# Kernel optimization log

Hardware: AMD Instinct MI355X
Metric: run time of the kernel (lower is better)

The kernel has to match this reference:

```python
import jax, jax.numpy as jnp
import numpy as np

B, V = 4, 10242
N = B * V            # 40968 packed vertices
E_PER = 30720        # edges per mesh
HID = 128


def _bilinear_sample(fm, grid):
    """pytorch3d vert_align core: grid_sample(align_corners=True, bilinear).
    fm: [B,C,H,W], grid: [B,V,2] xy in [-1,1] -> [B,V,C]."""
    b_, c_, h_, w_ = fm.shape
    x = (grid[..., 0] + 1.0) * 0.5 * (w_ - 1)
    y = (grid[..., 1] + 1.0) * 0.5 * (h_ - 1)
    x0f, y0f = jnp.floor(x), jnp.floor(y)
    wx1, wy1 = x - x0f, y - y0f
    wx0, wy0 = 1.0 - wx1, 1.0 - wy1
    x0 = jnp.clip(x0f, 0, w_ - 1).astype(jnp.int32)
    x1 = jnp.clip(x0f + 1, 0, w_ - 1).astype(jnp.int32)
    y0 = jnp.clip(y0f, 0, h_ - 1).astype(jnp.int32)
    y1 = jnp.clip(y0f + 1, 0, h_ - 1).astype(jnp.int32)
    fmt = jnp.transpose(fm, (0, 2, 3, 1))  # [B,H,W,C]
    bi = jnp.arange(b_)[:, None]
    g = lambda yy, xx: fmt[bi, yy, xx]     # [B,V,C]
    return ((wy0 * wx0)[..., None] * g(y0, x0)
            + (wy0 * wx1)[..., None] * g(y0, x1)
            + (wy1 * wx0)[..., None] * g(y1, x0)
            + (wy1 * wx1)[..., None] * g(y1, x1))


def _graph_conv(x, edges, w0, b0, w1, b1):
    """pytorch3d GraphConv (undirected): W0 x_i + sum over both edge dirs of W1 x_j."""
    h0 = x @ w0 + b0
    h1 = x @ w1 + b1
    e0, e1 = edges[:, 0], edges[:, 1]
    agg = jnp.zeros_like(h0).at[e0].add(h1[e1]).at[e1].add(h1[e0])
    return h0 + agg


def setup_inputs() -> dict:
    key = jax.random.key(0)
    ks = jax.random.split(key, 20)
    s = 0.05
    # per-mesh edges, offset into packed index space
    e = jax.random.randint(ks[0], (B, E_PER, 2), 0, V)
    e = e + (jnp.arange(B) * V)[:, None, None]
    return {
        "feat1": jax.random.normal(ks[1], (B, 256, 56, 56), jnp.float32),
        "feat2": jax.random.normal(ks[2], (B, 512, 28, 28), jnp.float32),
        "feat3": jax.random.normal(ks[3], (B, 1024, 14, 14), jnp.float32),
        "feat4": jax.random.normal(ks[4], (B, 2048, 7, 7), jnp.float32),
        "aligned_verts": jax.random.uniform(ks[5], (B, V, 3), jnp.float32, -1.0, 1.0),
        "verts_packed": jax.random.normal(ks[6], (N, 3), jnp.float32),
        "image_enc": jax.random.normal(ks[7], (B, 256), jnp.float32),
        "edges": e.reshape(B * E_PER, 2).astype(jnp.int64),
        "bottleneck_w": jax.random.normal(ks[8], (3840, HID), jnp.float32) * s,
        "bottleneck_b": jnp.zeros((HID,), jnp.float32),
        "g0_w0": jax.random.normal(ks[9], (387, HID), jnp.float32) * s,
        "g0_b0": jnp.zeros((HID,), jnp.float32),
        "g0_w1": jax.random.normal(ks[10], (387, HID), jnp.float32) * s,
        "g0_b1": jnp.zeros((HID,), jnp.float32),
        "gw0": jax.random.normal(ks[11], (7, HID, HID), jnp.float32) * s,
        "gb0": jnp.zeros((7, HID), jnp.float32),
        "gw1": jax.random.normal(ks[12], (7, HID, HID), jnp.float32) * s,
        "gb1": jnp.zeros((7, HID), jnp.float32),
        "off_w": jax.random.normal(ks[13], (HID, 3), jnp.float32) * s,
        "off_b": jnp.zeros((3,), jnp.float32),
    }


def reference(feat1, feat2, feat3, feat4, aligned_verts, verts_packed, image_enc,
              edges, bottleneck_w, bottleneck_b, g0_w0, g0_b0, g0_w1, g0_b1,
              gw0, gb0, gw1, gb1, off_w, off_b):
    grid = aligned_verts[..., :2]  # vert_align uses xy only
    samp = jnp.concatenate([_bilinear_sample(f, grid)
                            for f in (feat1, feat2, feat3, feat4)], axis=-1)
    samp = samp.reshape(N, 3840)  # return_packed=True
    vfeat = jax.nn.relu(samp @ bottleneck_w + bottleneck_b)
    enc = jnp.repeat(image_enc, V, axis=0)  # repeat_interleave
    x = jnp.concatenate([vfeat, verts_packed, enc], axis=1)  # [N,387]
    x = jax.nn.relu(_graph_conv(x, edges, g0_w0, g0_b0, g0_w1, g0_b1))
    for i in range(7):
        x = jax.nn.relu(_graph_conv(x, edges, gw0[i], gb0[i], gw1[i], gb1[i]))
    return x @ off_w + off_b  # delta_v [N,3]
```

## Files before the change

kernel.cpp:

```cpp
#include <hip/hip_runtime.h>

static inline int ceil_div(int a, int b) { return (a + b - 1) / b; }

typedef __attribute__((ext_vector_type(8))) short short8;
typedef __attribute__((ext_vector_type(4))) float floatx4;

__device__ __forceinline__ unsigned short f2bf(float f) {
    unsigned int u = __float_as_uint(f);
    unsigned int r = (u + 0x7fffu + ((u >> 16) & 1u)) >> 16;
    return (unsigned short)r;
}
__device__ __forceinline__ float bf2f(unsigned short h) {
    return __uint_as_float(((unsigned int)h) << 16);
}

__global__ __launch_bounds__(1024) void scan1_k(const int* __restrict__ deg,
                                                int* __restrict__ excl,
                                                int* __restrict__ bsum, int Nv) {
    __shared__ int s[1024];
    int tid = threadIdx.x;
    int i = blockIdx.x * 1024 + tid;
    int v = (i < Nv) ? deg[i] : 0;
    s[tid] = v;
    __syncthreads();
    for (int off = 1; off < 1024; off <<= 1) {
        int t = (tid >= off) ? s[tid - off] : 0;
        __syncthreads();
        if (tid >= off) s[tid] += t;
        __syncthreads();
    }
    if (i < Nv) excl[i] = s[tid] - v;
    if (tid == 1023) bsum[blockIdx.x] = s[1023];
}

__global__ __launch_bounds__(64) void scan2_k(int* __restrict__ bsum, int nb) {
    __shared__ int s[64];
    int tid = threadIdx.x;
    int v = (tid < nb) ? bsum[tid] : 0;
    s[tid] = v;
    __syncthreads();
    for (int off = 1; off < 64; off <<= 1) {
        int t = (tid >= off) ? s[tid - off] : 0;
        __syncthreads();
        if (tid >= off) s[tid] += t;
        __syncthreads();
    }
    if (tid < nb) bsum[tid] = s[tid] - v;
}

__global__ __launch_bounds__(1024) void scan3_k(const int* __restrict__ excl,
                                                const int* __restrict__ bsum,
                                                const int* __restrict__ deg,
                                                int* __restrict__ rowptr,
                                                int* __restrict__ cursor, int Nv) {
    int i = blockIdx.x * 1024 + threadIdx.x;
    if (i < Nv) {
        int val = excl[i] + bsum[blockIdx.x];
        rowptr[i] = val;
        cursor[i] = val;
        if (i == Nv - 1) rowptr[Nv] = val + deg[i];
    }
}

__global__ __launch_bounds__(256) void fill_adj_k(const int* __restrict__ edges,
                                                  int* __restrict__ cursor,
                                                  int* __restrict__ adj, int E) {
    int e = blockIdx.x * blockDim.x + threadIdx.x;
    if (e < E) {
        int a = edges[2 * e], b = edges[2 * e + 1];
        adj[atomicAdd(&cursor[a], 1)] = b;
        adj[atomicAdd(&cursor[b], 1)] = a;
    }
}

__global__ __launch_bounds__(256) void fatpre_k(const int* __restrict__ edges,
                                                int* __restrict__ deg, int E, int nE,
                                                const float* __restrict__ g0w0,
                                                const float* __restrict__ g0w1,
                                                const float* __restrict__ gw0,
                                                const float* __restrict__ gw1,
                                                unsigned short* __restrict__ Wt,
                                                const float* __restrict__ enc,
                                                float* __restrict__ encp, int B_) {
    int bid = blockIdx.x;
    int tid = threadIdx.x;
    if (bid < nE) {
        int e = bid * 256 + tid;
        if (e < E) {
            atomicAdd(&deg[edges[2 * e]], 1);
            atomicAdd(&deg[edges[2 * e + 1]], 1);
        }
    } else if (bid < nE + 16) {
        int lh = bid - nE;
        int l = lh >> 1, h = lh & 1;
        const float* src;
        if (l == 0) src = h ? g0w1 : g0w0;
        else src = (h ? gw1 : gw0) + (size_t)(l - 1) * 16384;
        unsigned short* dst = Wt + (size_t)lh * 16384;
        for (int idx = tid; idx < 16384; idx += 256) {
            int n = idx >> 7, k = idx & 127;
            dst[n * 128 + k] = f2bf(src[k * 128 + n]);
        }
    } else {
        int b = bid - nE - 16;
        int sH = tid >> 7;
        int j = tid & 127;
        const float* w = sH ? g0w1 : g0w0;
        const float* eb = enc + b * 256;
        float acc = 0.f;
        for (int c = 0; c < 256; ++c) acc = fmaf(eb[c], w[(131 + c) * 128 + j], acc);
        encp[(sH * B_ + b) * 128 + j] = acc;
    }
}

__global__ __launch_bounds__(256) void proj_all_k(
    const float* __restrict__ fm1, const float* __restrict__ fm2,
    const float* __restrict__ fm3, const float* __restrict__ fm4,
    const float* __restrict__ bw, float* __restrict__ q1, float* __restrict__ q2,
    float* __restrict__ q3, float* __restrict__ q4, int B_) {
    __shared__ float Xs[32][64];
    __shared__ float Ws[32][128];
    int tid = threadIdx.x;

    int n1 = 49 * B_ * 4, n2 = 13 * B_ * 8, n3 = 4 * B_ * 16;
    int bid = blockIdx.x;
    const float* fm;
    const float* W;
    float* op;
    int C, HW, PT, idx;
    if (bid < n1) {
        fm = fm1; W = bw; op = q1; C = 256; HW = 3136; PT = 49; idx = bid;
    } else if (bid < n1 + n2) {
        fm = fm2; W = bw + 256 * 128; op = q2; C = 512; HW = 784; PT = 13; idx = bid - n1;
    } else if (bid < n1 + n2 + n3) {
        fm = fm3; W = bw + 768 * 128; op = q3; C = 1024; HW = 196; PT = 4; idx = bid - n1 - n2;
    } else {
        fm = fm4; W = bw + 1792 * 128; op = q4; C = 2048; HW = 49; PT = 1;
        idx = bid - n1 - n2 - n3;
    }
    int pt = idx % PT;
    int r2 = idx / PT;
    int b = r2 % B_;
    int zz = r2 / B_;
    int p0 = pt * 64;
    int c0 = zz * 64;
    int S = B_ * HW * 128;
    const float* fmb = fm + (size_t)b * C * HW;

    float acc[8][4];
#pragma unroll
    for (int i = 0; i < 8; i++)
#pragma unroll
        for (int j = 0; j < 4; j++) acc[i][j] = 0.f;

    bool vec_ok = ((HW & 3) == 0);
    for (int kc = c0; kc < c0 + 64; kc += 32) {
        {
            int p4 = (tid & 15) * 4;
            int k0 = tid >> 4;
#pragma unroll
            for (int kk = 0; kk < 32; kk += 16) {
                int k = k0 + kk;
                const float* src = fmb + (size_t)(kc + k) * HW + p0 + p4;
                float4 v;
                if (vec_ok && (p0 + p4 + 3 < HW)) {
                    v = *(const float4*)src;
                } else {
                    v.x = (p0 + p4 + 0 < HW) ? src[0] : 0.f;
                    v.y = (p0 + p4 + 1 < HW) ? src[1] : 0.f;
                    v.z = (p0 + p4 + 2 < HW) ? src[2] : 0.f;
                    v.w = (p0 + p4 + 3 < HW) ? src[3] : 0.f;
                }
                *(float4*)&Xs[k][p4] = v;
            }
        }
        {
            int j4 = (tid & 31) * 4;
            int k0 = tid >> 5;
#pragma unroll
            for (int kk = 0; kk < 32; kk += 8) {
                int k = k0 + kk;
                *(float4*)&Ws[k][j4] = *(const float4*)(W + (size_t)(kc + k) * 128 + j4);
            }
        }
        __syncthreads();
        int rb = (tid >> 5) * 8;
        int cb = (tid & 31) * 4;
#pragma unroll 8
        for (int k = 0; k < 32; ++k) {
            float xr[8], wc[4];
#pragma unroll
            for (int i = 0; i < 8; i++) xr[i] = Xs[k][rb + i];
#pragma unroll
            for (int j = 0; j < 4; j++) wc[j] = Ws[k][cb + j];
#pragma unroll
            for (int i = 0; i < 8; i++)
#pragma unroll
                for (int j = 0; j < 4; j++) acc[i][j] = fmaf(xr[i], wc[j], acc[i][j]);
        }
        __syncthreads();
    }
    int rb = (tid >> 5) * 8;
    int cb = (tid & 31) * 4;
    float* obase = op + (size_t)zz * S;
#pragma unroll
    for (int i = 0; i < 8; i++) {
        int p = p0 + rb + i;
        if (p < HW) {
            *(float4*)(obase + ((size_t)b * HW + p) * 128 + cb) =
                make_float4(acc[i][0], acc[i][1], acc[i][2], acc[i][3]);
        }
    }
}

__global__ __launch_bounds__(256) void reduce4_k(const float* __restrict__ q1,
                                                 const float* __restrict__ q2,
                                                 const float* __restrict__ q3,
                                                 const float* __restrict__ q4,
                                                 float* __restrict__ o1, float* __restrict__ o2,
                                                 float* __restrict__ o3, float* __restrict__ o4,
                                                 int S1, int S2, int S3, int S4) {
    int i = (blockIdx.x * 256 + threadIdx.x) * 4;
    const float* src;
    float* dst;
    int S, z, base;
    if (i < S1) {
        src = q1; dst = o1; S = S1; z = 4; base = i;
    } else if (i < S1 + S2) {
        src = q2; dst = o2; S = S2; z = 8; base = i - S1;
    } else if (i < S1 + S2 + S3) {
        src = q3; dst = o3; S = S3; z = 16; base = i - S1 - S2;
    } else if (i < S1 + S2 + S3 + S4) {
        src = q4; dst = o4; S = S4; z = 32; base = i - S1 - S2 - S3;
    } else {
        return;
    }
    float4 a = *(const float4*)(src + base);
    for (int zz = 1; zz < z; ++zz) {
        float4 b = *(const float4*)(src + (size_t)zz * S + base);
        a.x += b.x; a.y += b.y; a.z += b.z; a.w += b.w;
    }
    *(float4*)(dst + base) = a;
}

__device__ __forceinline__ float sample_level(const float* __restrict__ pp, int Hh, int Ww,
                                              float gx, float gy, int j) {
    float x = (gx + 1.f) * 0.5f * (float)(Ww - 1);
    float y = (gy + 1.f) * 0.5f * (float)(Hh - 1);
    float x0f = floorf(x), y0f = floorf(y);
    float wx1 = x - x0f, wy1 = y - y0f;
    float wx0 = 1.f - wx1, wy0 = 1.f - wy1;
    int x0 = (int)fminf(fmaxf(x0f, 0.f), (float)(Ww - 1));
    int x1 = (int)fminf(fmaxf(x0f + 1.f, 0.f), (float)(Ww - 1));
    int y0 = (int)fminf(fmaxf(y0f, 0.f), (float)(Hh - 1));
    int y1 = (int)fminf(fmaxf(y0f + 1.f, 0.f), (float)(Hh - 1));
    const float* r00 = pp + (size_t)(y0 * Ww + x0) * 128;
    const float* r01 = pp + (size_t)(y0 * Ww + x1) * 128;
    const float* r10 = pp + (size_t)(y1 * Ww + x0) * 128;
    const float* r11 = pp + (size_t)(y1 * Ww + x1) * 128;
    return wy0 * (wx0 * r00[j] + wx1 * r01[j]) + wy1 * (wx0 * r10[j] + wx1 * r11[j]);
}

__global__ __launch_bounds__(128) void sample_bottleneck_k(
    const float* __restrict__ av, const float* __restrict__ pp1, const float* __restrict__ pp2,
    const float* __restrict__ pp3, const float* __restrict__ pp4, const float* __restrict__ bb,
    const float* __restrict__ verts, const float* __restrict__ encp,
    const float* __restrict__ g0w0, const float* __restrict__ g0w1,
    const float* __restrict__ g0b0, const float* __restrict__ g0b1,
    unsigned short* __restrict__ X, unsigned short* __restrict__ H, int V_, int B_) {
    int n = blockIdx.x, j = threadIdx.x;
    int b = n / V_;
    float gx = av[(size_t)n * 3 + 0];
    float gy = av[(size_t)n * 3 + 1];
    float acc = bb[j];
    acc += sample_level(pp1 + (size_t)b * 3136 * 128, 56, 56, gx, gy, j);
    acc += sample_level(pp2 + (size_t)b * 784 * 128, 28, 28, gx, gy, j);
    acc += sample_level(pp3 + (size_t)b * 196 * 128, 14, 14, gx, gy, j);
    acc += sample_level(pp4 + (size_t)b * 49 * 128, 7, 7, gx, gy, j);
    X[(size_t)n * 128 + j] = f2bf(fmaxf(acc, 0.f));
    float v0 = verts[n * 3 + 0], v1 = verts[n * 3 + 1], v2 = verts[n * 3 + 2];
    float h0 = encp[(0 * B_ + b) * 128 + j] + g0b0[j] + v0 * g0w0[128 * 128 + j] +
               v1 * g0w0[129 * 128 + j] + v2 * g0w0[130 * 128 + j];
    float h1 = encp[(1 * B_ + b) * 128 + j] + g0b1[j] + v0 * g0w1[128 * 128 + j] +
               v1 * g0w1[129 * 128 + j] + v2 * g0w1[130 * 128 + j];
    H[(size_t)n * 256 + j] = f2bf(h0);
    H[(size_t)n * 256 + 128 + j] = f2bf(h1);
}

__global__ __launch_bounds__(256) void aggpre_k(const unsigned short* __restrict__ H,
                                                const int* __restrict__ rowptr,
                                                const int* __restrict__ adj,
                                                float* __restrict__ pre, int Nv) {
    int wave = threadIdx.x >> 6, lane = threadIdx.x & 63;
    int n = blockIdx.x * 4 + wave;
    if (n >= Nv) return;
    unsigned int u = *(const unsigned int*)(H + (size_t)n * 256 + 2 * lane);
    float a0 = bf2f((unsigned short)(u & 0xffff));
    float a1 = bf2f((unsigned short)(u >> 16));
    int s = rowptr[n], e = rowptr[n + 1];
    for (int t = s; t < e; t += 8) {
        int nb[8];
        unsigned int w[8];
#pragma unroll
        for (int q = 0; q < 8; ++q) {
            int idx = (t + q < e) ? (t + q) : (e - 1);
            nb[q] = adj[idx];
        }
#pragma unroll
        for (int q = 0; q < 8; ++q)
            w[q] = *(const unsigned int*)(H + (size_t)nb[q] * 256 + 128 + 2 * lane);
#pragma unroll
        for (int q = 0; q < 8; ++q) {
            if (t + q < e) {
                a0 += bf2f((unsigned short)(w[q] & 0xffff));
                a1 += bf2f((unsigned short)(w[q] >> 16));
            }
        }
    }
    pre[(size_t)n * 128 + 2 * lane] = a0;
    pre[(size_t)n * 128 + 2 * lane + 1] = a1;
}

__global__ __launch_bounds__(256) void agg_x_k(const unsigned short* __restrict__ X,
                                               const int* __restrict__ rowptr,
                                               const int* __restrict__ adj,
                                               unsigned short* __restrict__ Agg, int Nv) {
    int wave = threadIdx.x >> 6, lane = threadIdx.x & 63;
    int n = blockIdx.x * 4 + wave;
    if (n >= Nv) return;
    const unsigned int* Xu = (const unsigned int*)X;
    float a0 = 0.f, a1 = 0.f;
    int s = rowptr[n], e = rowptr[n + 1];
    for (int t = s; t < e; t += 8) {
        int nb[8];
        unsigned int w[8];
#pragma unroll
        for (int q = 0; q < 8; ++q) {
            int idx = (t + q < e) ? (t + q) : (e - 1);
            nb[q] = adj[idx];
        }
#pragma unroll
        for (int q = 0; q < 8; ++q) w[q] = Xu[(size_t)nb[q] * 64 + lane];
#pragma unroll
        for (int q = 0; q < 8; ++q) {
            if (t + q < e) {
                a0 += bf2f((unsigned short)(w[q] & 0xffff));
                a1 += bf2f((unsigned short)(w[q] >> 16));
            }
        }
    }
    unsigned int o = (unsigned int)f2bf(a0) | ((unsigned int)f2bf(a1) << 16);
    *(unsigned int*)(Agg + (size_t)n * 128 + 2 * lane) = o;
}

__global__ __launch_bounds__(256, 3) void gemm_dual_k(
    const unsigned short* __restrict__ Xin, const unsigned short* __restrict__ Agg,
    const unsigned short* __restrict__ Wt,
    const float* __restrict__ b0, const float* __restrict__ b1,
    const float* __restrict__ pre, const int* __restrict__ degv,
    unsigned short* __restrict__ Xout, int M) {
    __shared__ unsigned short wlds[16384];
    __shared__ unsigned short cs[64 * 72];
    __shared__ float bS[128];

    int tid = threadIdx.x;
    int m0 = blockIdx.x * 128;
    int yb = blockIdx.y;

    int wave = tid >> 6, lane = tid & 63;
    int row16 = lane & 15;
    int quad = lane >> 4;
    int wrow = wave * 16;

    short8 axT[2][4], agT[2][4];
    int dgT[2][4];
    {
        int g = min(m0 + wrow + row16, M - 1);
#pragma unroll
        for (int ks = 0; ks < 4; ++ks) {
            int koff = ks * 32 + quad * 8;
            axT[0][ks] = *(const short8*)(Xin + (size_t)g * 128 + koff);
            agT[0][ks] = *(const short8*)(Agg + (size_t)g * 128 + koff);
        }
#pragma unroll
        for (int rr = 0; rr < 4; ++rr)
            dgT[0][rr] = degv[min(m0 + wrow + quad * 4 + rr, M - 1)];
    }

    if (tid < 64) {
        bS[tid] = b0 ? b0[yb * 64 + tid] : 0.f;
        bS[64 + tid] = b1 ? b1[yb * 64 + tid] : 0.f;
    }

    const unsigned short* W0h = Wt + (size_t)yb * 64 * 128;
    const unsigned short* W1h = Wt + 16384 + (size_t)yb * 64 * 128;
#pragma unroll
    for (int l = 0; l < 8; ++l) {
        int idx = tid + l * 256;
        int half = idx >> 10;
        int r = (idx >> 4) & 63;
        int c16 = idx & 15;
        int sw = (c16 ^ (r & 15)) * 8;
        const unsigned short* src = (half ? W1h : W0h) + r * 128 + c16 * 8;
        *(short8*)&wlds[half * 8192 + r * 128 + sw] = *(const short8*)src;
    }
    __syncthreads();

    {
        int g = min(m0 + 64 + wrow + row16, M - 1);
#pragma unroll
        for (int ks = 0; ks < 4; ++ks) {
            int koff = ks * 32 + quad * 8;
            axT[1][ks] = *(const short8*)(Xin + (size_t)g * 128 + koff);
            agT[1][ks] = *(const short8*)(Agg + (size_t)g * 128 + koff);
        }
#pragma unroll
        for (int rr = 0; rr < 4; ++rr)
            dgT[1][rr] = degv[min(m0 + 64 + wrow + quad * 4 + rr, M - 1)];
    }

#pragma unroll
    for (int t = 0; t < 2; ++t) {
        int mT = m0 + t * 64;
        floatx4 acc[4];
#pragma unroll
        for (int j = 0; j < 4; j++) acc[j] = (floatx4){0.f, 0.f, 0.f, 0.f};

#pragma unroll
        for (int ks = 0; ks < 4; ++ks) {
            int c = ks * 4 + quad;
#pragma unroll
            for (int nt = 0; nt < 4; ++nt) {
                int wr = nt * 16 + row16;
                short8 bw0 = *(short8*)&wlds[wr * 128 + ((c ^ row16) * 8)];
                short8 bw1 = *(short8*)&wlds[8192 + wr * 128 + ((c ^ row16) * 8)];
                acc[nt] = __builtin_amdgcn_mfma_f32_16x16x32_bf16(axT[t][ks], bw0, acc[nt], 0, 0, 0);
                acc[nt] = __builtin_amdgcn_mfma_f32_16x16x32_bf16(agT[t][ks], bw1, acc[nt], 0, 0, 0);
            }
        }

#pragma unroll
        for (int nt = 0; nt < 4; ++nt) {
            int colh = nt * 16 + row16;
            int colg = yb * 64 + colh;
            float bc0 = bS[colh];
            float bc1 = bS[64 + colh];
#pragma unroll
            for (int rr = 0; rr < 4; ++rr) {
                int row = wrow + quad * 4 + rr;
                int gm = mT + row;
                float v = acc[nt][rr] + bc0 + (float)dgT[t][rr] * bc1;
                if (pre && gm < M) v += pre[(size_t)gm * 128 + colg];
                cs[row * 72 + colh] = f2bf(fmaxf(v, 0.f));
            }
        }
        __syncthreads();

        {
            int r = tid >> 2;
            int cq = (tid & 3) * 16;
            int gm = mT + r;
            if (gm < M) {
                unsigned short* dst = Xout + (size_t)gm * 128 + yb * 64 + cq;
                *(short8*)dst = *(short8*)&cs[r * 72 + cq];
                *(short8*)(dst + 8) = *(short8*)&cs[r * 72 + cq + 8];
            }
        }
        __syncthreads();
    }
}

__global__ __launch_bounds__(256) void head_k(const unsigned short* __restrict__ X,
                                              const float* __restrict__ off_w,
                                              const float* __restrict__ off_b,
                                              float* __restrict__ out, int Nv) {
    int wave = threadIdx.x >> 6, lane = threadIdx.x & 63;
    int n = blockIdx.x * 4 + wave;
    if (n >= Nv) return;
    unsigned int u = *(const unsigned int*)(X + (size_t)n * 128 + 2 * lane);
    float x0 = bf2f((unsigned short)(u & 0xffff));
    float x1 = bf2f((unsigned short)(u >> 16));
    int c0 = 2 * lane, c1 = 2 * lane + 1;
    float p0 = x0 * off_w[c0 * 3 + 0] + x1 * off_w[c1 * 3 + 0];
    float p1 = x0 * off_w[c0 * 3 + 1] + x1 * off_w[c1 * 3 + 1];
    float p2 = x0 * off_w[c0 * 3 + 2] + x1 * off_w[c1 * 3 + 2];
#pragma unroll
    for (int m = 1; m < 64; m <<= 1) {
        p0 += __shfl_xor(p0, m);
        p1 += __shfl_xor(p1, m);
        p2 += __shfl_xor(p2, m);
    }
    if (lane == 0) {
        out[n * 3 + 0] = p0 + off_b[0];
        out[n * 3 + 1] = p1 + off_b[1];
        out[n * 3 + 2] = p2 + off_b[2];
    }
}

extern "C" void kernel_launch(void* const* d_in, const int* in_sizes, int n_in, void* d_out,
                              int out_size, void* d_ws, size_t ws_size, hipStream_t stream) {
    const float* feat1 = (const float*)d_in[0];
    const float* feat2 = (const float*)d_in[1];
    const float* feat3 = (const float*)d_in[2];
    const float* feat4 = (const float*)d_in[3];
    const float* av = (const float*)d_in[4];
    const float* verts = (const float*)d_in[5];
    const float* image_enc = (const float*)d_in[6];
    const int* edges = (const int*)d_in[7];
    const float* bw = (const float*)d_in[8];
    const float* bb = (const float*)d_in[9];
    const float* g0w0 = (const float*)d_in[10];
    const float* g0b0 = (const float*)d_in[11];
    const float* g0w1 = (const float*)d_in[12];
    const float* g0b1 = (const float*)d_in[13];
    const float* gw0 = (const float*)d_in[14];
    const float* gb0 = (const float*)d_in[15];
    const float* gw1 = (const float*)d_in[16];
    const float* gb1 = (const float*)d_in[17];
    const float* off_w = (const float*)d_in[18];
    const float* off_b = (const float*)d_in[19];

    int B_ = in_sizes[6] / 256;
    int N_ = in_sizes[5] / 3;
    int V_ = N_ / B_;
    int E_ = in_sizes[7] / 2;

    char* wsb = (char*)d_ws;
    size_t off = 0;
    auto alloc = [&](size_t bytes) -> void* {
        void* p = (void*)(wsb + off);
        off += (bytes + 255) & ~(size_t)255;
        return p;
    };
    int S1 = B_ * 3136 * 128;
    int S2 = B_ * 784 * 128;
    int S3 = B_ * 196 * 128;
    int S4 = B_ * 49 * 128;
    float* pp1 = (float*)alloc((size_t)S1 * 4);
    float* pp2 = (float*)alloc((size_t)S2 * 4);
    float* pp3 = (float*)alloc((size_t)S3 * 4);
    float* pp4 = (float*)alloc((size_t)S4 * 4);
    float* q1 = (float*)alloc((size_t)4 * S1 * 4);
    float* q2 = (float*)alloc((size_t)8 * S2 * 4);
    float* q3 = (float*)alloc((size_t)16 * S3 * 4);
    float* q4 = (float*)alloc((size_t)32 * S4 * 4);
    unsigned short* XA = (unsigned short*)alloc((size_t)N_ * 128 * 2);
    unsigned short* XB = (unsigned short*)alloc((size_t)N_ * 128 * 2);
    unsigned short* AggB = (unsigned short*)alloc((size_t)N_ * 128 * 2);
    unsigned short* Hb = (unsigned short*)alloc((size_t)N_ * 256 * 2);
    float* pre = (float*)alloc((size_t)N_ * 128 * 4);
    unsigned short* Wt = (unsigned short*)alloc((size_t)8 * 2 * 128 * 128 * 2);
    float* encp = (float*)alloc((size_t)2 * B_ * 128 * 4);
    int* deg = (int*)alloc((size_t)(N_ + 1) * 4);
    int* rowptr = (int*)alloc((size_t)(N_ + 1) * 4);
    int* cursor = (int*)alloc((size_t)N_ * 4);
    int* excl = (int*)alloc((size_t)N_ * 4);
    int* bsum = (int*)alloc((size_t)64 * 4);
    int* adj = (int*)alloc((size_t)2 * E_ * 4);

    hipMemsetAsync(deg, 0, (N_ + 1) * sizeof(int), stream);

    int nE = ceil_div(E_, 256);
    fatpre_k<<<nE + 16 + B_, 256, 0, stream>>>(edges, deg, E_, nE, g0w0, g0w1, gw0, gw1, Wt,
                                               image_enc, encp, B_);

    int nb = ceil_div(N_, 1024);
    scan1_k<<<nb, 1024, 0, stream>>>(deg, excl, bsum, N_);
    scan2_k<<<1, 64, 0, stream>>>(bsum, nb);
    scan3_k<<<nb, 1024, 0, stream>>>(excl, bsum, deg, rowptr, cursor, N_);
    fill_adj_k<<<ceil_div(E_, 256), 256, 0, stream>>>(edges, cursor, adj, E_);

    int nproj = 49 * B_ * 4 + 13 * B_ * 8 + 4 * B_ * 16 + 1 * B_ * 32;
    proj_all_k<<<nproj, 256, 0, stream>>>(feat1, feat2, feat3, feat4, bw, q1, q2, q3, q4, B_);
    int tot4 = (S1 + S2 + S3 + S4) / 4;
    reduce4_k<<<ceil_div(tot4, 256), 256, 0, stream>>>(q1, q2, q3, q4, pp1, pp2, pp3, pp4, S1,
                                                       S2, S3, S4);

    sample_bottleneck_k<<<N_, 128, 0, stream>>>(av, pp1, pp2, pp3, pp4, bb, verts, encp, g0w0,
                                                g0w1, g0b0, g0b1, XA, Hb, V_, B_);

    aggpre_k<<<ceil_div(N_, 4), 256, 0, stream>>>(Hb, rowptr, adj, pre, N_);

    int agrid = ceil_div(N_, 4);
    dim3 ggrid(ceil_div(N_, 128), 2);
    agg_x_k<<<agrid, 256, 0, stream>>>(XA, rowptr, adj, AggB, N_);
    gemm_dual_k<<<ggrid, 256, 0, stream>>>(XA, AggB, Wt, nullptr, nullptr, pre, deg, XB, N_);
    unsigned short* Xc = XB;
    unsigned short* Xn = XA;
    for (int i = 0; i < 7; ++i) {
        agg_x_k<<<agrid, 256, 0, stream>>>(Xc, rowptr, adj, AggB, N_);
        gemm_dual_k<<<ggrid, 256, 0, stream>>>(Xc, AggB, Wt + (size_t)(i + 1) * 32768,
                                               gb0 + i * 128, gb1 + i * 128, nullptr, deg, Xn,
                                               N_);
        unsigned short* t = Xc;
        Xc = Xn;
        Xn = t;
    }
    head_k<<<ceil_div(N_, 4), 256, 0, stream>>>(Xc, off_w, off_b, (float*)d_out, N_);
}
```

Measured before the change: 491.4 us.

## Fuse neighbor aggregation into the graph-conv GEMM kernel per layer

Merges the separate gather-aggregate kernel and the dual GEMM into a single layer kernel. Each 64-row block gathers neighbor sums straight into LDS, then runs both output-column halves itself, reloading weights for each half. This removes the intermediate Agg buffer round trip through global memory and one launch per layer. In exchange each block does more serial gather work per wave (16 rows per wave), loads weights twice, and uses more LDS, so occupancy drops to 2 blocks.

Result: slower. 762.2 us (+55.1%).

```diff
diff --git a/kernel.cpp b/kernel.cpp
--- a/kernel.cpp
+++ b/kernel.cpp
@@ -321,107 +321,89 @@
     pre[(size_t)n * 128 + 2 * lane + 1] = a1;
 }
 
-__global__ __launch_bounds__(256) void agg_x_k(const unsigned short* __restrict__ X,
-                                               const int* __restrict__ rowptr,
-                                               const int* __restrict__ adj,
-                                               unsigned short* __restrict__ Agg, int Nv) {
-    int wave = threadIdx.x >> 6, lane = threadIdx.x & 63;
-    int n = blockIdx.x * 4 + wave;
-    if (n >= Nv) return;
-    const unsigned int* Xu = (const unsigned int*)X;
-    float a0 = 0.f, a1 = 0.f;
-    int s = rowptr[n], e = rowptr[n + 1];
-    for (int t = s; t < e; t += 8) {
-        int nb[8];
-        unsigned int w[8];
-#pragma unroll
-        for (int q = 0; q < 8; ++q) {
-            int idx = (t + q < e) ? (t + q) : (e - 1);
-            nb[q] = adj[idx];
-        }
-#pragma unroll
-        for (int q = 0; q < 8; ++q) w[q] = Xu[(size_t)nb[q] * 64 + lane];
-#pragma unroll
-        for (int q = 0; q < 8; ++q) {
-            if (t + q < e) {
-                a0 += bf2f((unsigned short)(w[q] & 0xffff));
-                a1 += bf2f((unsigned short)(w[q] >> 16));
-            }
-        }
-    }
-    unsigned int o = (unsigned int)f2bf(a0) | ((unsigned int)f2bf(a1) << 16);
-    *(unsigned int*)(Agg + (size_t)n * 128 + 2 * lane) = o;
-}
-
-__global__ __launch_bounds__(256, 3) void gemm_dual_k(
-    const unsigned short* __restrict__ Xin, const unsigned short* __restrict__ Agg,
-    const unsigned short* __restrict__ Wt,
+__global__ __launch_bounds__(256, 2) void layer_k(
+    const unsigned short* __restrict__ Xin, const unsigned short* __restrict__ Wt,
     const float* __restrict__ b0, const float* __restrict__ b1,
     const float* __restrict__ pre, const int* __restrict__ degv,
+    const int* __restrict__ rowptr, const int* __restrict__ adj,
     unsigned short* __restrict__ Xout, int M) {
-    __shared__ unsigned short wlds[16384];
+    __shared__ unsigned short aggS[8192];
+    __shared__ unsigned short wS[16384];
     __shared__ unsigned short cs[64 * 72];
-    __shared__ float bS[128];
+    __shared__ float bS[256];
 
     int tid = threadIdx.x;
-    int m0 = blockIdx.x * 128;
-    int yb = blockIdx.y;
-
+    int m0 = blockIdx.x * 64;
     int wave = tid >> 6, lane = tid & 63;
-    int row16 = lane & 15;
-    int quad = lane >> 4;
+    int row16 = lane & 15, quad = lane >> 4;
     int wrow = wave * 16;
 
-    short8 axT[2][4], agT[2][4];
-    int dgT[2][4];
-    {
-        int g = min(m0 + wrow + row16, M - 1);
-#pragma unroll
-        for (int ks = 0; ks < 4; ++ks) {
-            int koff = ks * 32 + quad * 8;
-            axT[0][ks] = *(const short8*)(Xin + (size_t)g * 128 + koff);
-            agT[0][ks] = *(const short8*)(Agg + (size_t)g * 128 + koff);
-        }
-#pragma unroll
-        for (int rr = 0; rr < 4; ++rr)
-            dgT[0][rr] = degv[min(m0 + wrow + quad * 4 + rr, M - 1)];
-    }
-
-    if (tid < 64) {
-        bS[tid] = b0 ? b0[yb * 64 + tid] : 0.f;
-        bS[64 + tid] = b1 ? b1[yb * 64 + tid] : 0.f;
-    }
-
-    const unsigned short* W0h = Wt + (size_t)yb * 64 * 128;
-    const unsigned short* W1h = Wt + 16384 + (size_t)yb * 64 * 128;
-#pragma unroll
-    for (int l = 0; l < 8; ++l) {
-        int idx = tid + l * 256;
-        int half = idx >> 10;
-        int r = (idx >> 4) & 63;
-        int c16 = idx & 15;
-        int sw = (c16 ^ (r & 15)) * 8;
-        const unsigned short* src = (half ? W1h : W0h) + r * 128 + c16 * 8;
-        *(short8*)&wlds[half * 8192 + r * 128 + sw] = *(const short8*)src;
+    short8 ax[4];
+    int gA = min(m0 + wrow + row16, M - 1);
+#pragma unroll
+    for (int ks = 0; ks < 4; ++ks)
+        ax[ks] = *(const short8*)(Xin + (size_t)gA * 128 + ks * 32 + quad * 8);
+    int dg[4];
+#pragma unroll
+    for (int rr = 0; rr < 4; ++rr) dg[rr] = degv[min(m0 + wrow + quad * 4 + rr, M - 1)];
+
+    if (tid < 128) {
+        bS[tid] = b0 ? b0[tid] : 0.f;
+        bS[128 + tid] = b1 ? b1[tid] : 0.f;
+    }
+
+    const unsigned int* Xu = (const unsigned int*)Xin;
+    for (int r = wrow; r < wrow + 16; ++r) {
+        int n = m0 + r;
+        float a0 = 0.f, a1 = 0.f;
+        if (n < M) {
+            int s = rowptr[n], e = rowptr[n + 1];
+            for (int t = s; t < e; t += 8) {
+                int nb[8];
+                unsigned int w[8];
+#pragma unroll
+                for (int q = 0; q < 8; ++q) nb[q] = adj[(t + q < e) ? (t + q) : (e - 1)];
+#pragma unroll
+                for (int q = 0; q < 8; ++q) w[q] = Xu[(size_t)nb[q] * 64 + lane];
+#pragma unroll
+                for (int q = 0; q < 8; ++q) {
+                    if (t + q < e) {
+                        a0 += bf2f((unsigned short)(w[q] & 0xffff));
+                        a1 += bf2f((unsigned short)(w[q] >> 16));
+                    }
+                }
+            }
+        }
+        unsigned int o = (unsigned int)f2bf(a0) | ((unsigned int)f2bf(a1) << 16);
+        int idx = r * 128 + (((lane >> 2) ^ (r & 15)) * 8 + ((2 * lane) & 7));
+        *(unsigned int*)&aggS[idx] = o;
     }
     __syncthreads();
 
-    {
-        int g = min(m0 + 64 + wrow + row16, M - 1);
-#pragma unroll
-        for (int ks = 0; ks < 4; ++ks) {
-            int koff = ks * 32 + quad * 8;
-            axT[1][ks] = *(const short8*)(Xin + (size_t)g * 128 + koff);
-            agT[1][ks] = *(const short8*)(Agg + (size_t)g * 128 + koff);
-        }
-#pragma unroll
-        for (int rr = 0; rr < 4; ++rr)
-            dgT[1][rr] = degv[min(m0 + 64 + wrow + quad * 4 + rr, M - 1)];
-    }
-
-#pragma unroll
-    for (int t = 0; t < 2; ++t) {
-        int mT = m0 + t * 64;
+    short8 ag[4];
+#pragma unroll
+    for (int ks = 0; ks < 4; ++ks) {
+        int c = ks * 4 + quad;
+        ag[ks] = *(short8*)&aggS[(wrow + row16) * 128 + ((c ^ row16) * 8)];
+    }
+
+#pragma unroll
+    for (int yb = 0; yb < 2; ++yb) {
+        if (yb) __syncthreads();
+        const unsigned short* W0h = Wt + (size_t)yb * 64 * 128;
+        const unsigned short* W1h = Wt + 16384 + (size_t)yb * 64 * 128;
+#pragma unroll
+        for (int l = 0; l < 8; ++l) {
+            int idx = tid + l * 256;
+            int half = idx >> 10;
+            int r = (idx >> 4) & 63;
+            int c16 = idx & 15;
+            int sw = (c16 ^ (r & 15)) * 8;
+            *(short8*)&wS[half * 8192 + r * 128 + sw] =
+                *(const short8*)((half ? W1h : W0h) + r * 128 + c16 * 8);
+        }
+        __syncthreads();
+
         floatx4 acc[4];
 #pragma unroll
         for (int j = 0; j < 4; j++) acc[j] = (floatx4){0.f, 0.f, 0.f, 0.f};
@@ -432,24 +414,25 @@
 #pragma unroll
             for (int nt = 0; nt < 4; ++nt) {
                 int wr = nt * 16 + row16;
-                short8 bw0 = *(short8*)&wlds[wr * 128 + ((c ^ row16) * 8)];
-                short8 bw1 = *(short8*)&wlds[8192 + wr * 128 + ((c ^ row16) * 8)];
-                acc[nt] = __builtin_amdgcn_mfma_f32_16x16x32_bf16(axT[t][ks], bw0, acc[nt], 0, 0, 0);
-                acc[nt] = __builtin_amdgcn_mfma_f32_16x16x32_bf16(agT[t][ks], bw1, acc[nt], 0, 0, 0);
-            }
-        }
+                short8 bw0 = *(short8*)&wS[wr * 128 + ((c ^ row16) * 8)];
+                short8 bw1 = *(short8*)&wS[8192 + wr * 128 + ((c ^ row16) * 8)];
+                acc[nt] = __builtin_amdgcn_mfma_f32_16x16x32_bf16(ax[ks], bw0, acc[nt], 0, 0, 0);
+                acc[nt] = __builtin_amdgcn_mfma_f32_16x16x32_bf16(ag[ks], bw1, acc[nt], 0, 0, 0);
+            }
+        }
+        __syncthreads();
 
 #pragma unroll
         for (int nt = 0; nt < 4; ++nt) {
             int colh = nt * 16 + row16;
             int colg = yb * 64 + colh;
-            float bc0 = bS[colh];
-            float bc1 = bS[64 + colh];
+            float bc0 = bS[colg];
+            float bc1 = bS[128 + colg];
 #pragma unroll
             for (int rr = 0; rr < 4; ++rr) {
                 int row = wrow + quad * 4 + rr;
-                int gm = mT + row;
-                float v = acc[nt][rr] + bc0 + (float)dgT[t][rr] * bc1;
+                int gm = m0 + row;
+                float v = acc[nt][rr] + bc0 + (float)dg[rr] * bc1;
                 if (pre && gm < M) v += pre[(size_t)gm * 128 + colg];
                 cs[row * 72 + colh] = f2bf(fmaxf(v, 0.f));
             }
@@ -459,14 +442,13 @@
         {
             int r = tid >> 2;
             int cq = (tid & 3) * 16;
-            int gm = mT + r;
+            int gm = m0 + r;
             if (gm < M) {
                 unsigned short* dst = Xout + (size_t)gm * 128 + yb * 64 + cq;
                 *(short8*)dst = *(short8*)&cs[r * 72 + cq];
                 *(short8*)(dst + 8) = *(short8*)&cs[r * 72 + cq + 8];
             }
         }
-        __syncthreads();
     }
 }
 
@@ -546,7 +528,6 @@
     float* q4 = (float*)alloc((size_t)32 * S4 * 4);
     unsigned short* XA = (unsigned short*)alloc((size_t)N_ * 128 * 2);
     unsigned short* XB = (unsigned short*)alloc((size_t)N_ * 128 * 2);
-    unsigned short* AggB = (unsigned short*)alloc((size_t)N_ * 128 * 2);
     unsigned short* Hb = (unsigned short*)alloc((size_t)N_ * 256 * 2);
     float* pre = (float*)alloc((size_t)N_ * 128 * 4);
     unsigned short* Wt = (unsigned short*)alloc((size_t)8 * 2 * 128 * 128 * 2);
@@ -581,17 +562,13 @@
 
     aggpre_k<<<ceil_div(N_, 4), 256, 0, stream>>>(Hb, rowptr, adj, pre, N_);
 
-    int agrid = ceil_div(N_, 4);
-    dim3 ggrid(ceil_div(N_, 128), 2);
-    agg_x_k<<<agrid, 256, 0, stream>>>(XA, rowptr, adj, AggB, N_);
-    gemm_dual_k<<<ggrid, 256, 0, stream>>>(XA, AggB, Wt, nullptr, nullptr, pre, deg, XB, N_);
+    int lgrid = ceil_div(N_, 64);
+    layer_k<<<lgrid, 256, 0, stream>>>(XA, Wt, nullptr, nullptr, pre, deg, rowptr, adj, XB, N_);
     unsigned short* Xc = XB;
     unsigned short* Xn = XA;
     for (int i = 0; i < 7; ++i) {
-        agg_x_k<<<agrid, 256, 0, stream>>>(Xc, rowptr, adj, AggB, N_);
-        gemm_dual_k<<<ggrid, 256, 0, stream>>>(Xc, AggB, Wt + (size_t)(i + 1) * 32768,
-                                               gb0 + i * 128, gb1 + i * 128, nullptr, deg, Xn,
-                                               N_);
+        layer_k<<<lgrid, 256, 0, stream>>>(Xc, Wt + (size_t)(i + 1) * 32768, gb0 + i * 128,
+                                           gb1 + i * 128, nullptr, deg, rowptr, adj, Xn, N_);
         unsigned short* t = Xc;
         Xc = Xn;
         Xn = t;
```
